# Kernel optimization log

Hardware: AMD Instinct MI355X
Metric: run time of the kernel (lower is better)

Reference implementation:

```python
import jax, jax.numpy as jnp
import numpy as np
from jax import lax


def setup_inputs() -> dict:
    key = jax.random.key(0)
    ks = jax.random.split(key, 6)
    B, L, D, H, K = 32, 256, 16, 64, 5
    T = L - K + 1            # 252
    S = (T // 2) * H         # 8064
    return {
        "x": jax.random.normal(ks[0], (B, L, D), dtype=jnp.float32),
        "conv_w": jax.random.normal(ks[1], (D, H, K), dtype=jnp.float32) * 0.1,
        "conv_b": jax.random.normal(ks[2], (D, H), dtype=jnp.float32) * 0.1,
        "deconv_w": jax.random.normal(ks[3], (D, H, K), dtype=jnp.float32) * 0.1,
        "deconv_b": jax.random.normal(ks[4], (D,), dtype=jnp.float32) * 0.1,
        "W_attn": jax.random.normal(ks[5], (S, S), dtype=jnp.float32) * 0.01,
    }


def reference(x, conv_w, conv_b, deconv_w, deconv_b, W_attn):
    B, L, D = x.shape
    _, H, K = conv_w.shape
    T = L - K + 1
    P = T // 2
    S = P * H

    xt = jnp.transpose(x, (0, 2, 1))  # [B, D, L]
    # per-channel Conv1d(1->H) as one grouped conv: kernel [D*H, 1, K], groups=D
    y = lax.conv_general_dilated(
        xt, conv_w.reshape(D * H, 1, K), (1,), "VALID",
        dimension_numbers=("NCH", "OIH", "NCH"), feature_group_count=D,
    ) + conv_b.reshape(1, D * H, 1)
    y = jax.nn.relu(y)  # [B, D*H, T]

    # per-channel ConvTranspose1d(H->1) == full conv with flipped kernel, groups=D
    recon = lax.conv_general_dilated(
        y, deconv_w[..., ::-1], (1,), [(K - 1, K - 1)],
        dimension_numbers=("NCH", "OIH", "NCH"), feature_group_count=D,
    ) + deconv_b.reshape(1, D, 1)  # [B, D, L]

    # AvgPool1d(kernel=2, stride=2) then flatten(H, P) per channel
    pooled = y.reshape(B, D, H, P, 2).mean(axis=-1)  # [B, D, H, P]
    flat = pooled.reshape(B, D, S)                   # [B, D, S]

    main = flat[:, 0]        # [B, S]
    aux = flat[:, 1:]        # [B, D-1, S]

    # 'general' score: main . (aux @ W^T)  ==  (main @ W) . aux
    m = main @ W_attn                              # [B, S]
    scores = jnp.einsum("bt,bdt->bd", m, aux)      # [B, D-1]
    attn = jax.nn.softmax(scores, axis=-1)         # [B, D-1]
    weighted = jnp.einsum("bd,bds->bs", attn, aux)  # [B, S]

    out = jnp.concatenate([main[:, None, :], weighted[:, None, :]], axis=2)  # [B,1,2S]
    return out, attn[:, None, :], recon
```

## Files before the change

### kernel.cpp

```cpp
#include <hip/hip_runtime.h>
#include <math.h>

#define BB 32
#define LL 256
#define DD 16
#define HH 64
#define KK 5
#define TT 252
#define PP 126
#define SS 8064
#define NCHUNK 12
#define CHUNK 672
#define NKT 21

typedef __attribute__((ext_vector_type(8))) short bf16x8;
typedef __attribute__((ext_vector_type(4))) float f32x4;

__device__ __forceinline__ unsigned short f2bf(float f) {
  unsigned int u = __float_as_uint(f);
  u += 0x7FFFu + ((u >> 16) & 1u);
  return (unsigned short)(u >> 16);
}
__device__ __forceinline__ float bf2f(unsigned short h) {
  return __uint_as_float(((unsigned int)h) << 16);
}

__global__ __launch_bounds__(256) void k12_conv_recon(
    const float* __restrict__ x, const float* __restrict__ cw,
    const float* __restrict__ cb, const float* __restrict__ dw,
    const float* __restrict__ db, float* __restrict__ flat,
    unsigned short* __restrict__ mainH, unsigned short* __restrict__ mainL,
    float* __restrict__ recon) {
  __shared__ float ylds[HH * TT];
  __shared__ float xs[LL];
  __shared__ float cws[HH * KK];
  __shared__ float dws[HH * KK];
  __shared__ float cbs[HH];

  int bd = blockIdx.x;
  int b = bd / DD, d = bd % DD;
  int tid = threadIdx.x;

  xs[tid] = x[((size_t)b * LL + tid) * DD + d];
  for (int i = tid; i < HH * KK; i += 256) {
    cws[i] = cw[(size_t)d * HH * KK + i];
    dws[i] = dw[(size_t)d * HH * KK + i];
  }
  if (tid < HH) cbs[tid] = cb[d * HH + tid];
  __syncthreads();

  {
    int h = tid >> 2, a = tid & 3;
    int t0 = a * 63;
    float w0 = cws[h * KK + 0], w1 = cws[h * KK + 1], w2 = cws[h * KK + 2],
          w3 = cws[h * KK + 3], w4 = cws[h * KK + 4];
    float bias = cbs[h];
    float x0 = xs[t0], x1 = xs[t0 + 1], x2 = xs[t0 + 2], x3 = xs[t0 + 3],
          x4 = xs[t0 + 4];
    float* yrow = ylds + h * TT + t0;
    #pragma unroll 7
    for (int t = 0; t < 63; ++t) {
      float yv = fmaf(w4, x4, fmaf(w3, x3, fmaf(w2, x2, fmaf(w1, x1, fmaf(w0, x0, bias)))));
      yrow[t] = fmaxf(yv, 0.f);
      x0 = x1; x1 = x2; x2 = x3; x3 = x4;
      if (t < 62) x4 = xs[t0 + t + 5];
    }
  }
  __syncthreads();

  for (int i = tid; i < HH * PP; i += 256) {
    int h = i / PP, p = i - h * PP;
    float pooled = 0.5f * (ylds[h * TT + 2 * p] + ylds[h * TT + 2 * p + 1]);
    flat[(size_t)bd * SS + i] = pooled;
    if (d == 0) {
      unsigned short hb = f2bf(pooled);
      mainH[(size_t)b * SS + i] = hb;
      mainL[(size_t)b * SS + i] = f2bf(pooled - bf2f(hb));
    }
  }

  {
    int l = tid;
    float acc = db[d];
    for (int h = 0; h < HH; ++h) {
      const float* yl = ylds + h * TT;
      #pragma unroll
      for (int j = 0; j < KK; ++j) {
        int t = l - j;
        if (t >= 0 && t < TT) acc = fmaf(yl[t], dws[h * KK + j], acc);
      }
    }
    recon[(size_t)bd * LL + l] = acc;
  }
}

__global__ __launch_bounds__(256) void k3_mfma(
    const float* __restrict__ W, const unsigned short* __restrict__ mainH,
    const unsigned short* __restrict__ mainL, float* __restrict__ partial) {
  __shared__ unsigned short AH[2][1024];
  __shared__ unsigned short AL[2][1024];
  __shared__ unsigned short BH[2][4096];
  __shared__ unsigned short BL[2][4096];

  int tid = threadIdx.x;
  int chunk = blockIdx.y;
  int s0 = chunk * CHUNK;
  int cbase = blockIdx.x * 128;

  int lane = tid & 63;
  int wv = tid >> 6;
  int mr = wv & 1;
  int ctb = (wv >> 1) * 4;

  f32x4 c0 = {0.f, 0.f, 0.f, 0.f};
  f32x4 c1 = {0.f, 0.f, 0.f, 0.f};
  f32x4 c2 = {0.f, 0.f, 0.f, 0.f};
  f32x4 c3 = {0.f, 0.f, 0.f, 0.f};

  int sc2 = (tid & 63) * 2;
  int sg = tid >> 6;
  const float* wbase = W + (size_t)(s0 + sg * 8) * SS + cbase + sc2;

  int ab = tid >> 2, aq = tid & 3;
  size_t abase = (size_t)ab * SS + (size_t)(s0 + aq * 8);

  int aoff  = (lane >> 4) * 256 + ((lane & 15) + 16 * mr) * 8;
  int boff0 = (lane >> 4) * 1024 + ((ctb) * 16 + (lane & 15)) * 8;

  float2 e0, e1, e2, e3, e4, e5, e6, e7;
  float2 o0, o1, o2, o3, o4, o5, o6, o7;
  bf16x8 aEH, aEL, aOH, aOL;

#define LOADW(R0,R1,R2,R3,R4,R5,R6,R7, KT) {                          \
    const float* p_ = wbase + (size_t)(KT) * 32 * SS;                 \
    R0 = *(const float2*)(p_);                                        \
    R1 = *(const float2*)(p_ + (size_t)SS);                           \
    R2 = *(const float2*)(p_ + 2 * (size_t)SS);                       \
    R3 = *(const float2*)(p_ + 3 * (size_t)SS);                       \
    R4 = *(const float2*)(p_ + 4 * (size_t)SS);                       \
    R5 = *(const float2*)(p_ + 5 * (size_t)SS);                       \
    R6 = *(const float2*)(p_ + 6 * (size_t)SS);                       \
    R7 = *(const float2*)(p_ + 7 * (size_t)SS); }

#define LOADA(RH, RL, KT) if (tid < 128) {                            \
    RH = *(const bf16x8*)(mainH + abase + (KT) * 32);                 \
    RL = *(const bf16x8*)(mainL + abase + (KT) * 32); }

#define SPLITC(F, J) {                                                \
    unsigned int ux_ = __float_as_uint(F.x);                          \
    unsigned int uy_ = __float_as_uint(F.y);                          \
    h0[J] = (short)(ux_ >> 16); h1[J] = (short)(uy_ >> 16);           \
    float rx_ = F.x - __uint_as_float(ux_ & 0xFFFF0000u);             \
    float ry_ = F.y - __uint_as_float(uy_ & 0xFFFF0000u);             \
    l0[J] = (short)(__float_as_uint(rx_) >> 16);                      \
    l1[J] = (short)(__float_as_uint(ry_) >> 16); }

#define CVTW(R0,R1,R2,R3,R4,R5,R6,R7, BUF) {                          \
    bf16x8 h0, h1, l0, l1;                                            \
    SPLITC(R0, 0) SPLITC(R1, 1) SPLITC(R2, 2) SPLITC(R3, 3)           \
    SPLITC(R4, 4) SPLITC(R5, 5) SPLITC(R6, 6) SPLITC(R7, 7)           \
    *(bf16x8*)&BH[BUF][sg * 1024 + sc2 * 8]     = h0;                 \
    *(bf16x8*)&BH[BUF][sg * 1024 + sc2 * 8 + 8] = h1;                 \
    *(bf16x8*)&BL[BUF][sg * 1024 + sc2 * 8]     = l0;                 \
    *(bf16x8*)&BL[BUF][sg * 1024 + sc2 * 8 + 8] = l1; }

#define WRITEA(RH, RL, BUF) if (tid < 128) {                          \
    *(bf16x8*)&AH[BUF][aq * 256 + ab * 8] = RH;                       \
    *(bf16x8*)&AL[BUF][aq * 256 + ab * 8] = RL; }

#define DOMFMA(BUF) {                                                 \
    bf16x8 ah  = *(const bf16x8*)&AH[BUF][aoff];                      \
    bf16x8 al  = *(const bf16x8*)&AL[BUF][aoff];                      \
    bf16x8 bh0 = *(const bf16x8*)&BH[BUF][boff0];                     \
    bf16x8 bl0 = *(const bf16x8*)&BL[BUF][boff0];                     \
    bf16x8 bh1 = *(const bf16x8*)&BH[BUF][boff0 + 128];               \
    bf16x8 bl1 = *(const bf16x8*)&BL[BUF][boff0 + 128];               \
    bf16x8 bh2 = *(const bf16x8*)&BH[BUF][boff0 + 256];               \
    bf16x8 bl2 = *(const bf16x8*)&BL[BUF][boff0 + 256];               \
    bf16x8 bh3 = *(const bf16x8*)&BH[BUF][boff0 + 384];               \
    bf16x8 bl3 = *(const bf16x8*)&BL[BUF][boff0 + 384];               \
    c0 = __builtin_amdgcn_mfma_f32_16x16x32_bf16(ah, bh0, c0, 0, 0, 0); \
    c0 = __builtin_amdgcn_mfma_f32_16x16x32_bf16(ah, bl0, c0, 0, 0, 0); \
    c0 = __builtin_amdgcn_mfma_f32_16x16x32_bf16(al, bh0, c0, 0, 0, 0); \
    c1 = __builtin_amdgcn_mfma_f32_16x16x32_bf16(ah, bh1, c1, 0, 0, 0); \
    c1 = __builtin_amdgcn_mfma_f32_16x16x32_bf16(ah, bl1, c1, 0, 0, 0); \
    c1 = __builtin_amdgcn_mfma_f32_16x16x32_bf16(al, bh1, c1, 0, 0, 0); \
    c2 = __builtin_amdgcn_mfma_f32_16x16x32_bf16(ah, bh2, c2, 0, 0, 0); \
    c2 = __builtin_amdgcn_mfma_f32_16x16x32_bf16(ah, bl2, c2, 0, 0, 0); \
    c2 = __builtin_amdgcn_mfma_f32_16x16x32_bf16(al, bh2, c2, 0, 0, 0); \
    c3 = __builtin_amdgcn_mfma_f32_16x16x32_bf16(ah, bh3, c3, 0, 0, 0); \
    c3 = __builtin_amdgcn_mfma_f32_16x16x32_bf16(ah, bl3, c3, 0, 0, 0); \
    c3 = __builtin_amdgcn_mfma_f32_16x16x32_bf16(al, bh3, c3, 0, 0, 0); }

  LOADW(e0,e1,e2,e3,e4,e5,e6,e7, 0) LOADA(aEH, aEL, 0)
  CVTW(e0,e1,e2,e3,e4,e5,e6,e7, 0) WRITEA(aEH, aEL, 0)
  LOADW(o0,o1,o2,o3,o4,o5,o6,o7, 1) LOADA(aOH, aOL, 1)
  __syncthreads();

  #pragma unroll 1
  for (int kt = 0; kt < NKT - 1; kt += 2) {
    LOADW(e0,e1,e2,e3,e4,e5,e6,e7, kt + 2) LOADA(aEH, aEL, kt + 2)
    DOMFMA(0)
    CVTW(o0,o1,o2,o3,o4,o5,o6,o7, 1) WRITEA(aOH, aOL, 1)
    __syncthreads();
    if (kt + 3 < NKT) {
      LOADW(o0,o1,o2,o3,o4,o5,o6,o7, kt + 3) LOADA(aOH, aOL, kt + 3)
    }
    DOMFMA(1)
    CVTW(e0,e1,e2,e3,e4,e5,e6,e7, 0) WRITEA(aEH, aEL, 0)
    __syncthreads();
  }
  DOMFMA(0)

  int row0 = mr * 16 + (lane >> 4) * 4;
  int col0 = cbase + ctb * 16 + (lane & 15);
  float* pp = partial + ((size_t)chunk * BB + row0) * SS + col0;
  #pragma unroll
  for (int r = 0; r < 4; ++r) pp[(size_t)r * SS]      = c0[r];
  #pragma unroll
  for (int r = 0; r < 4; ++r) pp[(size_t)r * SS + 16] = c1[r];
  #pragma unroll
  for (int r = 0; r < 4; ++r) pp[(size_t)r * SS + 32] = c2[r];
  #pragma unroll
  for (int r = 0; r < 4; ++r) pp[(size_t)r * SS + 48] = c3[r];
#undef LOADW
#undef LOADA
#undef SPLITC
#undef CVTW
#undef WRITEA
#undef DOMFMA
}

__global__ __launch_bounds__(256) void k3b_reduce(
    const float4* __restrict__ partial, float4* __restrict__ m) {
  int i = blockIdx.x * 256 + threadIdx.x;
  float4 s = make_float4(0.f, 0.f, 0.f, 0.f);
  #pragma unroll
  for (int c = 0; c < NCHUNK; ++c) {
    float4 v = partial[(size_t)c * (BB * SS / 4) + i];
    s.x += v.x; s.y += v.y; s.z += v.z; s.w += v.w;
  }
  m[i] = s;
}

__global__ __launch_bounds__(256) void k4_scores(
    const float* __restrict__ m, const float* __restrict__ flat,
    float* __restrict__ scores) {
  int bd = blockIdx.x;
  int b = bd / 15, dd = bd % 15;
  const float* mb = m + (size_t)b * SS;
  const float* ab = flat + ((size_t)b * DD + 1 + dd) * SS;
  float p = 0.f;
  for (int s = threadIdx.x; s < SS; s += 256) p = fmaf(mb[s], ab[s], p);
  #pragma unroll
  for (int o = 32; o; o >>= 1) p += __shfl_xor(p, o);
  __shared__ float red[4];
  if ((threadIdx.x & 63) == 0) red[threadIdx.x >> 6] = p;
  __syncthreads();
  if (threadIdx.x == 0) scores[bd] = red[0] + red[1] + red[2] + red[3];
}

__global__ __launch_bounds__(64) void k5_softmax(
    const float* __restrict__ scores, float* __restrict__ attn_out) {
  int b = blockIdx.x;
  int lane = threadIdx.x;
  float v = (lane < 15) ? scores[b * 15 + lane] : -INFINITY;
  float mx = v;
  #pragma unroll
  for (int o = 32; o; o >>= 1) mx = fmaxf(mx, __shfl_xor(mx, o));
  float e = (lane < 15) ? expf(v - mx) : 0.f;
  float sum = e;
  #pragma unroll
  for (int o = 32; o; o >>= 1) sum += __shfl_xor(sum, o);
  if (lane < 15) attn_out[b * 15 + lane] = e / sum;
}

__global__ __launch_bounds__(256) void k6_out(
    const float* __restrict__ flat, const float* __restrict__ attn,
    float* __restrict__ out) {
  int b = blockIdx.y;
  int s = blockIdx.x * 256 + threadIdx.x;
  if (s >= SS) return;
  const float* fb = flat + (size_t)b * DD * SS;
  out[(size_t)b * 2 * SS + s] = fb[s];
  float w = 0.f;
  #pragma unroll
  for (int d = 0; d < 15; ++d)
    w = fmaf(attn[b * 15 + d], fb[(size_t)(1 + d) * SS + s], w);
  out[(size_t)b * 2 * SS + SS + s] = w;
}

extern "C" void kernel_launch(void* const* d_in, const int* in_sizes, int n_in,
                              void* d_out, int out_size, void* d_ws, size_t ws_size,
                              hipStream_t stream) {
  const float* x        = (const float*)d_in[0];
  const float* conv_w   = (const float*)d_in[1];
  const float* conv_b   = (const float*)d_in[2];
  const float* deconv_w = (const float*)d_in[3];
  const float* deconv_b = (const float*)d_in[4];
  const float* W_attn   = (const float*)d_in[5];
  float* out = (float*)d_out;

  const size_t ATTN_OFF  = (size_t)BB * 2 * SS;
  const size_t RECON_OFF = ATTN_OFF + (size_t)BB * 15;

  float* ws      = (float*)d_ws;
  float* partial = ws;
  float* flat    = partial + (size_t)NCHUNK * BB * SS;
  unsigned short* mainH = (unsigned short*)(flat + (size_t)BB * DD * SS);
  unsigned short* mainL = mainH + (size_t)BB * SS;
  float* m       = (float*)(mainL + (size_t)BB * SS);
  float* scores  = m + (size_t)BB * SS;

  k12_conv_recon<<<dim3(BB * DD), dim3(256), 0, stream>>>(
      x, conv_w, conv_b, deconv_w, deconv_b, flat, mainH, mainL, out + RECON_OFF);

  k3_mfma<<<dim3(SS / 128, NCHUNK), dim3(256), 0, stream>>>(
      W_attn, mainH, mainL, partial);

  k3b_reduce<<<dim3((BB * SS / 4) / 256), dim3(256), 0, stream>>>(
      (const float4*)partial, (float4*)m);

  k4_scores<<<dim3(BB * 15), dim3(256), 0, stream>>>(m, flat, scores);

  k5_softmax<<<dim3(BB), dim3(64), 0, stream>>>(scores, out + ATTN_OFF);

  k6_out<<<dim3((SS + 255) / 256, BB), dim3(256), 0, stream>>>(
      flat, out + ATTN_OFF, out);
}
```

Baseline: 97.98 us.

## Drop W low-part split, prefragment A operands, and rebalance K chunks

The W operand is now converted to a single rounded bf16 instead of a hi/lo pair, which cuts MFMA count per tile from 12 to 8 and halves B-side LDS traffic. A new kernel pre-arranges the main vector's hi/lo bf16 fragments into MFMA lane order, so the GEMM loads A straight from global into registers with no LDS staging. K is split into 21 chunks of 384 rather than 12 of 672, giving more blocks but more partial sums to reduce. Dropping W's low part lowers the precision of main @ W, which may affect accuracy tolerance.

```diff
diff --git a/kernel.cpp b/kernel.cpp
--- a/kernel.cpp
+++ b/kernel.cpp
@@ -9,9 +9,10 @@
 #define TT 252
 #define PP 126
 #define SS 8064
-#define NCHUNK 12
-#define CHUNK 672
-#define NKT 21
+#define NCHUNK 21
+#define CHUNK 384
+#define NKT 12
+#define NGT 252
 
 typedef __attribute__((ext_vector_type(8))) short bf16x8;
 typedef __attribute__((ext_vector_type(4))) float f32x4;
@@ -94,13 +95,23 @@
   }
 }
 
+__global__ __launch_bounds__(256) void k2c_afrag(
+    const unsigned short* __restrict__ mainH,
+    const unsigned short* __restrict__ mainL,
+    unsigned short* __restrict__ afragH, unsigned short* __restrict__ afragL) {
+  int i = blockIdx.x * 256 + threadIdx.x;
+  int gt = i >> 7;
+  int r = i & 127;
+  int mr = r >> 6, l = r & 63;
+  size_t src = (size_t)(mr * 16 + (l & 15)) * SS + gt * 32 + (l >> 4) * 8;
+  *(bf16x8*)&afragH[(size_t)i * 8] = *(const bf16x8*)(mainH + src);
+  *(bf16x8*)&afragL[(size_t)i * 8] = *(const bf16x8*)(mainL + src);
+}
+
 __global__ __launch_bounds__(256) void k3_mfma(
-    const float* __restrict__ W, const unsigned short* __restrict__ mainH,
-    const unsigned short* __restrict__ mainL, float* __restrict__ partial) {
-  __shared__ unsigned short AH[2][1024];
-  __shared__ unsigned short AL[2][1024];
+    const float* __restrict__ W, const unsigned short* __restrict__ afragH,
+    const unsigned short* __restrict__ afragL, float* __restrict__ partial) {
   __shared__ unsigned short BH[2][4096];
-  __shared__ unsigned short BL[2][4096];
 
   int tid = threadIdx.x;
   int chunk = blockIdx.y;
@@ -121,11 +132,12 @@
   int sg = tid >> 6;
   const float* wbase = W + (size_t)(s0 + sg * 8) * SS + cbase + sc2;
 
-  int ab = tid >> 2, aq = tid & 3;
-  size_t abase = (size_t)ab * SS + (size_t)(s0 + aq * 8);
-
-  int aoff  = (lane >> 4) * 256 + ((lane & 15) + 16 * mr) * 8;
-  int boff0 = (lane >> 4) * 1024 + ((ctb) * 16 + (lane & 15)) * 8;
+  int boff0 = (lane >> 4) * 1024 + (ctb * 16 + (lane & 15)) * 8;
+
+  const unsigned short* afHb =
+      afragH + ((size_t)((chunk * NKT) * 2 + mr) * 64 + lane) * 8;
+  const unsigned short* afLb =
+      afragL + ((size_t)((chunk * NKT) * 2 + mr) * 64 + lane) * 8;
 
   float2 e0, e1, e2, e3, e4, e5, e6, e7;
   float2 o0, o1, o2, o3, o4, o5, o6, o7;
@@ -142,75 +154,54 @@
     R6 = *(const float2*)(p_ + 6 * (size_t)SS);                       \
     R7 = *(const float2*)(p_ + 7 * (size_t)SS); }
 
-#define LOADA(RH, RL, KT) if (tid < 128) {                            \
-    RH = *(const bf16x8*)(mainH + abase + (KT) * 32);                 \
-    RL = *(const bf16x8*)(mainL + abase + (KT) * 32); }
-
-#define SPLITC(F, J) {                                                \
-    unsigned int ux_ = __float_as_uint(F.x);                          \
-    unsigned int uy_ = __float_as_uint(F.y);                          \
-    h0[J] = (short)(ux_ >> 16); h1[J] = (short)(uy_ >> 16);           \
-    float rx_ = F.x - __uint_as_float(ux_ & 0xFFFF0000u);             \
-    float ry_ = F.y - __uint_as_float(uy_ & 0xFFFF0000u);             \
-    l0[J] = (short)(__float_as_uint(rx_) >> 16);                      \
-    l1[J] = (short)(__float_as_uint(ry_) >> 16); }
+#define LOADA(RH, RL, KT) {                                           \
+    RH = *(const bf16x8*)(afHb + (size_t)(KT) * 1024);                \
+    RL = *(const bf16x8*)(afLb + (size_t)(KT) * 1024); }
+
+#define CVT1(F, J) {                                                  \
+    h0[J] = (short)f2bf(F.x);                                         \
+    h1[J] = (short)f2bf(F.y); }
 
 #define CVTW(R0,R1,R2,R3,R4,R5,R6,R7, BUF) {                          \
-    bf16x8 h0, h1, l0, l1;                                            \
-    SPLITC(R0, 0) SPLITC(R1, 1) SPLITC(R2, 2) SPLITC(R3, 3)           \
-    SPLITC(R4, 4) SPLITC(R5, 5) SPLITC(R6, 6) SPLITC(R7, 7)           \
+    bf16x8 h0, h1;                                                    \
+    CVT1(R0, 0) CVT1(R1, 1) CVT1(R2, 2) CVT1(R3, 3)                   \
+    CVT1(R4, 4) CVT1(R5, 5) CVT1(R6, 6) CVT1(R7, 7)                   \
     *(bf16x8*)&BH[BUF][sg * 1024 + sc2 * 8]     = h0;                 \
-    *(bf16x8*)&BH[BUF][sg * 1024 + sc2 * 8 + 8] = h1;                 \
-    *(bf16x8*)&BL[BUF][sg * 1024 + sc2 * 8]     = l0;                 \
-    *(bf16x8*)&BL[BUF][sg * 1024 + sc2 * 8 + 8] = l1; }
-
-#define WRITEA(RH, RL, BUF) if (tid < 128) {                          \
-    *(bf16x8*)&AH[BUF][aq * 256 + ab * 8] = RH;                       \
-    *(bf16x8*)&AL[BUF][aq * 256 + ab * 8] = RL; }
-
-#define DOMFMA(BUF) {                                                 \
-    bf16x8 ah  = *(const bf16x8*)&AH[BUF][aoff];                      \
-    bf16x8 al  = *(const bf16x8*)&AL[BUF][aoff];                      \
+    *(bf16x8*)&BH[BUF][sg * 1024 + sc2 * 8 + 8] = h1; }
+
+#define DOMFMA(BUF, AH_, AL_) {                                       \
     bf16x8 bh0 = *(const bf16x8*)&BH[BUF][boff0];                     \
-    bf16x8 bl0 = *(const bf16x8*)&BL[BUF][boff0];                     \
     bf16x8 bh1 = *(const bf16x8*)&BH[BUF][boff0 + 128];               \
-    bf16x8 bl1 = *(const bf16x8*)&BL[BUF][boff0 + 128];               \
     bf16x8 bh2 = *(const bf16x8*)&BH[BUF][boff0 + 256];               \
-    bf16x8 bl2 = *(const bf16x8*)&BL[BUF][boff0 + 256];               \
     bf16x8 bh3 = *(const bf16x8*)&BH[BUF][boff0 + 384];               \
-    bf16x8 bl3 = *(const bf16x8*)&BL[BUF][boff0 + 384];               \
-    c0 = __builtin_amdgcn_mfma_f32_16x16x32_bf16(ah, bh0, c0, 0, 0, 0); \
-    c0 = __builtin_amdgcn_mfma_f32_16x16x32_bf16(ah, bl0, c0, 0, 0, 0); \
-    c0 = __builtin_amdgcn_mfma_f32_16x16x32_bf16(al, bh0, c0, 0, 0, 0); \
-    c1 = __builtin_amdgcn_mfma_f32_16x16x32_bf16(ah, bh1, c1, 0, 0, 0); \
-    c1 = __builtin_amdgcn_mfma_f32_16x16x32_bf16(ah, bl1, c1, 0, 0, 0); \
-    c1 = __builtin_amdgcn_mfma_f32_16x16x32_bf16(al, bh1, c1, 0, 0, 0); \
-    c2 = __builtin_amdgcn_mfma_f32_16x16x32_bf16(ah, bh2, c2, 0, 0, 0); \
-    c2 = __builtin_amdgcn_mfma_f32_16x16x32_bf16(ah, bl2, c2, 0, 0, 0); \
-    c2 = __builtin_amdgcn_mfma_f32_16x16x32_bf16(al, bh2, c2, 0, 0, 0); \
-    c3 = __builtin_amdgcn_mfma_f32_16x16x32_bf16(ah, bh3, c3, 0, 0, 0); \
-    c3 = __builtin_amdgcn_mfma_f32_16x16x32_bf16(ah, bl3, c3, 0, 0, 0); \
-    c3 = __builtin_amdgcn_mfma_f32_16x16x32_bf16(al, bh3, c3, 0, 0, 0); }
-
-  LOADW(e0,e1,e2,e3,e4,e5,e6,e7, 0) LOADA(aEH, aEL, 0)
-  CVTW(e0,e1,e2,e3,e4,e5,e6,e7, 0) WRITEA(aEH, aEL, 0)
-  LOADW(o0,o1,o2,o3,o4,o5,o6,o7, 1) LOADA(aOH, aOL, 1)
+    c0 = __builtin_amdgcn_mfma_f32_16x16x32_bf16(AH_, bh0, c0, 0, 0, 0); \
+    c0 = __builtin_amdgcn_mfma_f32_16x16x32_bf16(AL_, bh0, c0, 0, 0, 0); \
+    c1 = __builtin_amdgcn_mfma_f32_16x16x32_bf16(AH_, bh1, c1, 0, 0, 0); \
+    c1 = __builtin_amdgcn_mfma_f32_16x16x32_bf16(AL_, bh1, c1, 0, 0, 0); \
+    c2 = __builtin_amdgcn_mfma_f32_16x16x32_bf16(AH_, bh2, c2, 0, 0, 0); \
+    c2 = __builtin_amdgcn_mfma_f32_16x16x32_bf16(AL_, bh2, c2, 0, 0, 0); \
+    c3 = __builtin_amdgcn_mfma_f32_16x16x32_bf16(AH_, bh3, c3, 0, 0, 0); \
+    c3 = __builtin_amdgcn_mfma_f32_16x16x32_bf16(AL_, bh3, c3, 0, 0, 0); }
+
+  LOADW(e0,e1,e2,e3,e4,e5,e6,e7, 0)
+  CVTW(e0,e1,e2,e3,e4,e5,e6,e7, 0)
+  LOADW(o0,o1,o2,o3,o4,o5,o6,o7, 1)
+  LOADA(aEH, aEL, 0)
   __syncthreads();
 
   #pragma unroll 1
-  for (int kt = 0; kt < NKT - 1; kt += 2) {
-    LOADW(e0,e1,e2,e3,e4,e5,e6,e7, kt + 2) LOADA(aEH, aEL, kt + 2)
-    DOMFMA(0)
-    CVTW(o0,o1,o2,o3,o4,o5,o6,o7, 1) WRITEA(aOH, aOL, 1)
+  for (int kt = 0; kt < NKT; kt += 2) {
+    if (kt + 2 < NKT) LOADW(e0,e1,e2,e3,e4,e5,e6,e7, kt + 2)
+    LOADA(aOH, aOL, kt + 1)
+    DOMFMA(0, aEH, aEL)
+    CVTW(o0,o1,o2,o3,o4,o5,o6,o7, 1)
     __syncthreads();
-    if (kt + 3 < NKT) {
-      LOADW(o0,o1,o2,o3,o4,o5,o6,o7, kt + 3) LOADA(aOH, aOL, kt + 3)
-    }
-    DOMFMA(1)
-    CVTW(e0,e1,e2,e3,e4,e5,e6,e7, 0) WRITEA(aEH, aEL, 0)
+    if (kt + 3 < NKT) LOADW(o0,o1,o2,o3,o4,o5,o6,o7, kt + 3)
+    if (kt + 2 < NKT) LOADA(aEH, aEL, kt + 2)
+    DOMFMA(1, aOH, aOL)
+    if (kt + 2 < NKT) CVTW(e0,e1,e2,e3,e4,e5,e6,e7, 0)
     __syncthreads();
   }
-  DOMFMA(0)
 
   int row0 = mr * 16 + (lane >> 4) * 4;
   int col0 = cbase + ctb * 16 + (lane & 15);
@@ -225,9 +216,8 @@
   for (int r = 0; r < 4; ++r) pp[(size_t)r * SS + 48] = c3[r];
 #undef LOADW
 #undef LOADA
-#undef SPLITC
+#undef CVT1
 #undef CVTW
-#undef WRITEA
 #undef DOMFMA
 }
 
@@ -307,16 +297,21 @@
   float* ws      = (float*)d_ws;
   float* partial = ws;
   float* flat    = partial + (size_t)NCHUNK * BB * SS;
-  unsigned short* mainH = (unsigned short*)(flat + (size_t)BB * DD * SS);
-  unsigned short* mainL = mainH + (size_t)BB * SS;
-  float* m       = (float*)(mainL + (size_t)BB * SS);
+  unsigned short* mainH  = (unsigned short*)(flat + (size_t)BB * DD * SS);
+  unsigned short* mainL  = mainH + (size_t)BB * SS;
+  unsigned short* afragH = mainL + (size_t)BB * SS;
+  unsigned short* afragL = afragH + (size_t)NGT * 2 * 64 * 8;
+  float* m       = (float*)(afragL + (size_t)NGT * 2 * 64 * 8);
   float* scores  = m + (size_t)BB * SS;
 
   k12_conv_recon<<<dim3(BB * DD), dim3(256), 0, stream>>>(
       x, conv_w, conv_b, deconv_w, deconv_b, flat, mainH, mainL, out + RECON_OFF);
 
+  k2c_afrag<<<dim3((NGT * 2 * 64) / 256), dim3(256), 0, stream>>>(
+      mainH, mainL, afragH, afragL);
+
   k3_mfma<<<dim3(SS / 128, NCHUNK), dim3(256), 0, stream>>>(
-      W_attn, mainH, mainL, partial);
+      W_attn, afragH, afragL, partial);
 
   k3b_reduce<<<dim3((BB * SS / 4) / 256), dim3(256), 0, stream>>>(
       (const float4*)partial, (float4*)m);
```

New measurement: 108.4 us. 10.7% more time.

## Drop low bf16 half of W in split-precision MFMA and rechunk K dimension

Applied to the files above, without the earlier changes.

W is now converted to a single round-to-nearest bf16 value instead of a hi/lo pair, which removes the BL shared buffer, its stores and loads, and one third of the MFMAs. The K split changes from 12 chunks of 672 to 21 chunks of 384, giving more blocks for parallelism at the cost of more partial sums for the reduce kernel to read. The loop is restructured for an even tile count. The kernel is probably bound by reading W from memory, and the change lowers the precision of the main @ W product.

```diff
diff --git a/kernel.cpp b/kernel.cpp
--- a/kernel.cpp
+++ b/kernel.cpp
@@ -9,9 +9,9 @@
 #define TT 252
 #define PP 126
 #define SS 8064
-#define NCHUNK 12
-#define CHUNK 672
-#define NKT 21
+#define NCHUNK 21
+#define CHUNK 384
+#define NKT 12
 
 typedef __attribute__((ext_vector_type(8))) short bf16x8;
 typedef __attribute__((ext_vector_type(4))) float f32x4;
@@ -100,7 +100,6 @@
   __shared__ unsigned short AH[2][1024];
   __shared__ unsigned short AL[2][1024];
   __shared__ unsigned short BH[2][4096];
-  __shared__ unsigned short BL[2][4096];
 
   int tid = threadIdx.x;
   int chunk = blockIdx.y;
@@ -125,7 +124,7 @@
   size_t abase = (size_t)ab * SS + (size_t)(s0 + aq * 8);
 
   int aoff  = (lane >> 4) * 256 + ((lane & 15) + 16 * mr) * 8;
-  int boff0 = (lane >> 4) * 1024 + ((ctb) * 16 + (lane & 15)) * 8;
+  int boff0 = (lane >> 4) * 1024 + (ctb * 16 + (lane & 15)) * 8;
 
   float2 e0, e1, e2, e3, e4, e5, e6, e7;
   float2 o0, o1, o2, o3, o4, o5, o6, o7;
@@ -146,23 +145,16 @@
     RH = *(const bf16x8*)(mainH + abase + (KT) * 32);                 \
     RL = *(const bf16x8*)(mainL + abase + (KT) * 32); }
 
-#define SPLITC(F, J) {                                                \
-    unsigned int ux_ = __float_as_uint(F.x);                          \
-    unsigned int uy_ = __float_as_uint(F.y);                          \
-    h0[J] = (short)(ux_ >> 16); h1[J] = (short)(uy_ >> 16);           \
-    float rx_ = F.x - __uint_as_float(ux_ & 0xFFFF0000u);             \
-    float ry_ = F.y - __uint_as_float(uy_ & 0xFFFF0000u);             \
-    l0[J] = (short)(__float_as_uint(rx_) >> 16);                      \
-    l1[J] = (short)(__float_as_uint(ry_) >> 16); }
+#define CVT1(F, J) {                                                  \
+    h0[J] = (short)f2bf(F.x);                                         \
+    h1[J] = (short)f2bf(F.y); }
 
 #define CVTW(R0,R1,R2,R3,R4,R5,R6,R7, BUF) {                          \
-    bf16x8 h0, h1, l0, l1;                                            \
-    SPLITC(R0, 0) SPLITC(R1, 1) SPLITC(R2, 2) SPLITC(R3, 3)           \
-    SPLITC(R4, 4) SPLITC(R5, 5) SPLITC(R6, 6) SPLITC(R7, 7)           \
+    bf16x8 h0, h1;                                                    \
+    CVT1(R0, 0) CVT1(R1, 1) CVT1(R2, 2) CVT1(R3, 3)                   \
+    CVT1(R4, 4) CVT1(R5, 5) CVT1(R6, 6) CVT1(R7, 7)                   \
     *(bf16x8*)&BH[BUF][sg * 1024 + sc2 * 8]     = h0;                 \
-    *(bf16x8*)&BH[BUF][sg * 1024 + sc2 * 8 + 8] = h1;                 \
-    *(bf16x8*)&BL[BUF][sg * 1024 + sc2 * 8]     = l0;                 \
-    *(bf16x8*)&BL[BUF][sg * 1024 + sc2 * 8 + 8] = l1; }
+    *(bf16x8*)&BH[BUF][sg * 1024 + sc2 * 8 + 8] = h1; }
 
 #define WRITEA(RH, RL, BUF) if (tid < 128) {                          \
     *(bf16x8*)&AH[BUF][aq * 256 + ab * 8] = RH;                       \
@@ -172,24 +164,16 @@
     bf16x8 ah  = *(const bf16x8*)&AH[BUF][aoff];                      \
     bf16x8 al  = *(const bf16x8*)&AL[BUF][aoff];                      \
     bf16x8 bh0 = *(const bf16x8*)&BH[BUF][boff0];                     \
-    bf16x8 bl0 = *(const bf16x8*)&BL[BUF][boff0];                     \
     bf16x8 bh1 = *(const bf16x8*)&BH[BUF][boff0 + 128];               \
-    bf16x8 bl1 = *(const bf16x8*)&BL[BUF][boff0 + 128];               \
     bf16x8 bh2 = *(const bf16x8*)&BH[BUF][boff0 + 256];               \
-    bf16x8 bl2 = *(const bf16x8*)&BL[BUF][boff0 + 256];               \
     bf16x8 bh3 = *(const bf16x8*)&BH[BUF][boff0 + 384];               \
-    bf16x8 bl3 = *(const bf16x8*)&BL[BUF][boff0 + 384];               \
     c0 = __builtin_amdgcn_mfma_f32_16x16x32_bf16(ah, bh0, c0, 0, 0, 0); \
-    c0 = __builtin_amdgcn_mfma_f32_16x16x32_bf16(ah, bl0, c0, 0, 0, 0); \
     c0 = __builtin_amdgcn_mfma_f32_16x16x32_bf16(al, bh0, c0, 0, 0, 0); \
     c1 = __builtin_amdgcn_mfma_f32_16x16x32_bf16(ah, bh1, c1, 0, 0, 0); \
-    c1 = __builtin_amdgcn_mfma_f32_16x16x32_bf16(ah, bl1, c1, 0, 0, 0); \
     c1 = __builtin_amdgcn_mfma_f32_16x16x32_bf16(al, bh1, c1, 0, 0, 0); \
     c2 = __builtin_amdgcn_mfma_f32_16x16x32_bf16(ah, bh2, c2, 0, 0, 0); \
-    c2 = __builtin_amdgcn_mfma_f32_16x16x32_bf16(ah, bl2, c2, 0, 0, 0); \
     c2 = __builtin_amdgcn_mfma_f32_16x16x32_bf16(al, bh2, c2, 0, 0, 0); \
     c3 = __builtin_amdgcn_mfma_f32_16x16x32_bf16(ah, bh3, c3, 0, 0, 0); \
-    c3 = __builtin_amdgcn_mfma_f32_16x16x32_bf16(ah, bl3, c3, 0, 0, 0); \
     c3 = __builtin_amdgcn_mfma_f32_16x16x32_bf16(al, bh3, c3, 0, 0, 0); }
 
   LOADW(e0,e1,e2,e3,e4,e5,e6,e7, 0) LOADA(aEH, aEL, 0)
@@ -198,19 +182,16 @@
   __syncthreads();
 
   #pragma unroll 1
-  for (int kt = 0; kt < NKT - 1; kt += 2) {
-    LOADW(e0,e1,e2,e3,e4,e5,e6,e7, kt + 2) LOADA(aEH, aEL, kt + 2)
+  for (int kt = 0; kt < NKT; kt += 2) {
+    if (kt + 2 < NKT) { LOADW(e0,e1,e2,e3,e4,e5,e6,e7, kt + 2) LOADA(aEH, aEL, kt + 2) }
     DOMFMA(0)
     CVTW(o0,o1,o2,o3,o4,o5,o6,o7, 1) WRITEA(aOH, aOL, 1)
     __syncthreads();
-    if (kt + 3 < NKT) {
-      LOADW(o0,o1,o2,o3,o4,o5,o6,o7, kt + 3) LOADA(aOH, aOL, kt + 3)
-    }
+    if (kt + 3 < NKT) { LOADW(o0,o1,o2,o3,o4,o5,o6,o7, kt + 3) LOADA(aOH, aOL, kt + 3) }
     DOMFMA(1)
-    CVTW(e0,e1,e2,e3,e4,e5,e6,e7, 0) WRITEA(aEH, aEL, 0)
+    if (kt + 2 < NKT) { CVTW(e0,e1,e2,e3,e4,e5,e6,e7, 0) WRITEA(aEH, aEL, 0) }
     __syncthreads();
   }
-  DOMFMA(0)
 
   int row0 = mr * 16 + (lane >> 4) * 4;
   int col0 = cbase + ctb * 16 + (lane & 15);
@@ -225,7 +206,7 @@
   for (int r = 0; r < 4; ++r) pp[(size_t)r * SS + 48] = c3[r];
 #undef LOADW
 #undef LOADA
-#undef SPLITC
+#undef CVT1
 #undef CVTW
 #undef WRITEA
 #undef DOMFMA
```

Measured after the change: 104.2 us. 1.06x slower.
